# Performance work log

Measured on AMD Instinct MI355X. Metric: run time of the kernel, lower is better.

The kernel has to match this reference:

```python
import jax, jax.numpy as jnp
import numpy as np

BETA = 0.95
NUM_STEPS = 32


def setup_inputs() -> dict:
    key = jax.random.key(0)
    ks = jax.random.split(key, 6)
    B, IN, D, P = 1024, 512, 256, 8
    total = D * P
    x = jax.random.normal(ks[0], (B, IN), jnp.float32)
    W_proj = jax.random.normal(ks[1], (IN, total), jnp.float32) / np.sqrt(IN)
    b_proj = jnp.zeros((total,), jnp.float32)
    # uniform threshold distribution, sorted: linspace(0.5, 2.0, P)
    thresholds = jnp.linspace(0.5, 2.0, P, dtype=jnp.float32)
    rate_W = jax.random.normal(ks[2], (P, 1), jnp.float32) / np.sqrt(P)
    rate_b = jnp.zeros((1,), jnp.float32)
    conv1_w = jax.random.normal(ks[3], (P // 2, P, 3), jnp.float32) / np.sqrt(P * 3)
    conv1_b = jnp.zeros((P // 2,), jnp.float32)
    conv2_w = jax.random.normal(ks[4], (1, P // 2, 1), jnp.float32) / np.sqrt(P // 2)
    conv2_b = jnp.zeros((1,), jnp.float32)
    fusion = jnp.array([0.6, 0.4], jnp.float32)
    return dict(x=x, W_proj=W_proj, b_proj=b_proj, thresholds=thresholds,
                rate_W=rate_W, rate_b=rate_b, conv1_w=conv1_w, conv1_b=conv1_b,
                conv2_w=conv2_w, conv2_b=conv2_b, fusion=fusion)


def _conv1d(x, w, b):
    # x: [N, C_in, T], w: [C_out, C_in, K] -> [N, C_out, T] (SAME padding)
    y = jax.lax.conv_general_dilated(x, w, window_strides=(1,), padding='SAME',
                                     dimension_numbers=('NCH', 'OIH', 'NCH'))
    return y + b[None, :, None]


def reference(x, W_proj, b_proj, thresholds, rate_W, rate_b,
              conv1_w, conv1_b, conv2_w, conv2_b, fusion):
    B = x.shape[0]
    P = thresholds.shape[0]
    D = W_proj.shape[1] // P
    # constant input current per neuron: [B, D, P]
    I = (x @ W_proj + b_proj).reshape(B, D, P)

    # LIF recurrence (snntorch Leaky, reset_mechanism='subtract'):
    #   reset = H(mem_prev - thr); mem = beta*mem_prev + I - reset*thr; spk = H(mem - thr)
    def step(mem, _):
        reset = (mem > thresholds).astype(mem.dtype)
        mem = BETA * mem + I - reset * thresholds
        spk = (mem > thresholds).astype(mem.dtype)
        return mem, spk

    mem0 = jnp.zeros((B, D, P), x.dtype)
    _, spikes = jax.lax.scan(step, mem0, None, length=NUM_STEPS)  # [T, B, D, P]

    # rate branch
    rates = spikes.mean(axis=0)                        # [B, D, P]
    rate_dec = (rates @ rate_W)[..., 0] + rate_b[0]    # [B, D]

    # temporal branch: [B*D, P, T]
    s = jnp.transpose(spikes, (1, 2, 3, 0)).reshape(B * D, P, NUM_STEPS)
    h = jax.nn.relu(_conv1d(s, conv1_w, conv1_b))
    h = _conv1d(h, conv2_w, conv2_b)                   # [B*D, 1, T]
    temp_dec = h.mean(axis=-1).reshape(B, D)

    fw = jax.nn.softmax(fusion)
    return fw[0] * rate_dec + fw[1] * temp_dec
```

## Files before the change

kernel.cpp:

```cpp
#include <hip/hip_runtime.h>
#include <type_traits>


constexpr int IN_DIM  = 512;
constexpr int D_DIM   = 256;
constexpr int NTOT    = 2048;
constexpr int T_STEPS = 32;

constexpr int TM = 64;
constexpr int TN = 64;
constexpr int TK = 32;
constexpr int NSPLIT = 4;
constexpr int KSPLIT = IN_DIM / NSPLIT;

__global__ __launch_bounds__(128, 2)
void popcode_gemm(const float* __restrict__ x,
                  const float* __restrict__ Wp,
                  float* __restrict__ ws)
{
    __shared__ float As[TK][TM + 4];
    __shared__ float Bs[TK][TN];

    const int tid = threadIdx.x;
    const int b0  = blockIdx.x * TM;
    const int c0  = blockIdx.y * TN;
    const int k0  = blockIdx.z * KSPLIT;
    const int rg  = tid >> 3;
    const int dl  = tid & 7;
    const int r4  = rg * 4;

    float acc[4][8];
#pragma unroll
    for (int i = 0; i < 4; ++i)
#pragma unroll
        for (int j = 0; j < 8; ++j) acc[i][j] = 0.f;

    for (int kc = k0; kc < k0 + KSPLIT; kc += TK) {
#pragma unroll
        for (int i = 0; i < 4; ++i) {
            const int f   = tid + 128 * i;
            const int row = f >> 3;
            const int c4  = (f & 7) * 4;
            const float4 v =
                *reinterpret_cast<const float4*>(x + (b0 + row) * IN_DIM + kc + c4);
            As[c4 + 0][row] = v.x;
            As[c4 + 1][row] = v.y;
            As[c4 + 2][row] = v.z;
            As[c4 + 3][row] = v.w;
        }
#pragma unroll
        for (int i = 0; i < 4; ++i) {
            const int f  = tid + 128 * i;
            const int r  = f >> 4;
            const int c4 = (f & 15) * 4;
            *reinterpret_cast<float4*>(&Bs[r][c4]) =
                *reinterpret_cast<const float4*>(Wp + (kc + r) * NTOT + c0 + c4);
        }
        __syncthreads();

#pragma unroll 16
        for (int k = 0; k < TK; ++k) {
            const float4 a = *reinterpret_cast<const float4*>(&As[k][r4]);
            const float4 u = *reinterpret_cast<const float4*>(&Bs[k][dl * 8]);
            const float4 v = *reinterpret_cast<const float4*>(&Bs[k][dl * 8 + 4]);
            const float ar[4] = {a.x, a.y, a.z, a.w};
#pragma unroll
            for (int r = 0; r < 4; ++r) {
                acc[r][0] += ar[r] * u.x;  acc[r][1] += ar[r] * u.y;
                acc[r][2] += ar[r] * u.z;  acc[r][3] += ar[r] * u.w;
                acc[r][4] += ar[r] * v.x;  acc[r][5] += ar[r] * v.y;
                acc[r][6] += ar[r] * v.z;  acc[r][7] += ar[r] * v.w;
            }
        }
        __syncthreads();
    }

    float* dst = ws + (size_t)blockIdx.z * 1024 * NTOT;
#pragma unroll
    for (int bi = 0; bi < 4; ++bi) {
        float* p = dst + (size_t)(b0 + r4 + bi) * NTOT + c0 + dl * 8;
        *reinterpret_cast<float4*>(p)     = {acc[bi][0], acc[bi][1], acc[bi][2], acc[bi][3]};
        *reinterpret_cast<float4*>(p + 4) = {acc[bi][4], acc[bi][5], acc[bi][6], acc[bi][7]};
    }
}

__global__ __launch_bounds__(256)
void popcode_epi(const float* __restrict__ ws,
                 const float* __restrict__ bp,
                 const float* __restrict__ thrs,
                 const float* __restrict__ rateW,
                 const float* __restrict__ rateB,
                 const float* __restrict__ c1w,
                 const float* __restrict__ c1b,
                 const float* __restrict__ c2w,
                 const float* __restrict__ c2b,
                 const float* __restrict__ fus,
                 float* __restrict__ out)
{
    __shared__ float lut[3][256][4];
    __shared__ float rlut[256];
    __shared__ float wlds[96];
    __shared__ uint4 exch[256];

    const int tid = threadIdx.x;
    const int wv  = tid >> 6;
    const int h   = wv & 1;
    const int nl  = ((wv >> 1) << 6) | (tid & 63);
    const int n   = blockIdx.x * 128 + nl;
    const int b   = n >> 8;
    const int d   = n & 255;

    if (tid < 96) wlds[tid] = c1w[tid];
    {
        float rv = 0.f;
#pragma unroll
        for (int p = 0; p < 8; ++p)
            rv += (float)((tid >> p) & 1) * rateW[p];
        rlut[tid] = rv;
    }
    __syncthreads();
#pragma unroll
    for (int i = 0; i < 12; ++i) {
        const int e    = 256 * i + tid;
        const int k    = e >> 10;
        const int byte = (e >> 2) & 255;
        const int c    = e & 3;
        float v = (k == 1) ? c1b[c] : 0.f;
#pragma unroll
        for (int p = 0; p < 8; ++p)
            v = fmaf((float)((byte >> p) & 1), wlds[(c * 8 + p) * 3 + k], v);
        (&lut[0][0][0])[e] = v;
    }

    float w2c[4];
#pragma unroll
    for (int c = 0; c < 4; ++c) w2c[c] = c2w[c];
    const float rb_ = rateB[0];
    const float bb2 = c2b[0];
    const float f0 = fus[0], f1 = fus[1];
    const float fm = fmaxf(f0, f1);
    const float e0 = __expf(f0 - fm), e1 = __expf(f1 - fm);
    const float inv = 1.f / (e0 + e1);
    const float fw0 = e0 * inv, fw1 = e1 * inv;

    const size_t base  = (size_t)b * NTOT + d * 8 + h * 4;
    const size_t slice = (size_t)1024 * NTOT;
    float4 iv = *reinterpret_cast<const float4*>(ws + base);
#pragma unroll
    for (int s = 1; s < NSPLIT; ++s) {
        const float4 q = *reinterpret_cast<const float4*>(ws + s * slice + base);
        iv.x += q.x; iv.y += q.y; iv.z += q.z; iv.w += q.w;
    }
    const float4 bpv = *reinterpret_cast<const float4*>(bp + d * 8 + h * 4);
    const float4 tv  = *reinterpret_cast<const float4*>(thrs + h * 4);
    float Iv[4]  = {iv.x + bpv.x, iv.y + bpv.y, iv.z + bpv.z, iv.w + bpv.w};
    float thr[4] = {tv.x, tv.y, tv.z, tv.w};
    float Imt[4], mem[4];
    bool  spk[4];
#pragma unroll
    for (int p = 0; p < 4; ++p) {
        Imt[p] = Iv[p] - thr[p];
        mem[p] = 0.f;
        spk[p] = false;
    }

    unsigned nib[4] = {0u, 0u, 0u, 0u};
#pragma unroll
    for (int t = 0; t < T_STEPS; ++t) {
        unsigned nb = 0u;
#pragma unroll
        for (int p = 0; p < 4; ++p) {
            mem[p] = 0.95f * mem[p] + (spk[p] ? Imt[p] : Iv[p]);
            spk[p] = mem[p] > thr[p];
            nb |= spk[p] ? (1u << p) : 0u;
        }
        nib[t >> 3] |= nb << (4 * (t & 7));
    }

    __syncthreads();
    exch[tid] = uint4{nib[0], nib[1], nib[2], nib[3]};
    __syncthreads();
    const uint4 pr = exch[tid ^ 64];
    const unsigned prn[4] = {pr.x, pr.y, pr.z, pr.w};
    unsigned lo[4], hi[4];
#pragma unroll
    for (int w = 0; w < 4; ++w) {
        lo[w] = h ? prn[w] : nib[w];
        hi[w] = h ? nib[w] : prn[w];
    }

    auto getbyte = [&](int t) -> unsigned {
        const int w = t >> 3, s = 4 * (t & 7);
        return ((lo[w] >> s) & 15u) | (((hi[w] >> s) & 15u) << 4);
    };
    const float* lutf = &lut[0][0][0];
    float tacc = 0.f, rsum = 0.f;

    auto conv_half = [&](auto T0C) {
        constexpr int T0 = T0C.value;
        unsigned bprev = (T0 == 0) ? 0u : getbyte(T0 - 1);
        unsigned bcur  = getbyte(T0);
#pragma unroll
        for (int i = 0; i < 16; ++i) {
            const int t = T0 + i;
            const unsigned bnext = (t < 31) ? getbyte(t + 1) : 0u;
            const float4 fa = *reinterpret_cast<const float4*>(lutf + bprev * 4);
            const float4 fb = *reinterpret_cast<const float4*>(lutf + 1024 + bcur * 4);
            const float4 fc = *reinterpret_cast<const float4*>(lutf + 2048 + bnext * 4);
            rsum += rlut[bcur];
            const float h0_ = (fa.x + fb.x) + fc.x;
            const float h1_ = (fa.y + fb.y) + fc.y;
            const float h2_ = (fa.z + fb.z) + fc.z;
            const float h3_ = (fa.w + fb.w) + fc.w;
            tacc = fmaf(fmaxf(h0_, 0.f), w2c[0], tacc);
            tacc = fmaf(fmaxf(h1_, 0.f), w2c[1], tacc);
            tacc = fmaf(fmaxf(h2_, 0.f), w2c[2], tacc);
            tacc = fmaf(fmaxf(h3_, 0.f), w2c[3], tacc);
            bprev = bcur;
            bcur  = bnext;
        }
    };
    if (h == 0) conv_half(std::integral_constant<int, 0>{});
    else        conv_half(std::integral_constant<int, 16>{});

    __syncthreads();
    float2* e2 = reinterpret_cast<float2*>(exch);
    e2[tid] = float2{rsum, tacc};
    __syncthreads();
    const float2 q = e2[tid ^ 64];
    rsum += q.x;
    tacc += q.y;

    if (h == 0) {
        const float rdec = rsum * (1.f / 32.f) + rb_;
        const float temp = tacc * (1.f / 32.f) + bb2;
        out[b * D_DIM + d] = fw0 * rdec + fw1 * temp;
    }
}

extern "C" void kernel_launch(void* const* d_in, const int* in_sizes, int n_in,
                              void* d_out, int out_size, void* d_ws, size_t ws_size,
                              hipStream_t stream) {
    const float* x     = (const float*)d_in[0];
    const float* Wp    = (const float*)d_in[1];
    const float* bp    = (const float*)d_in[2];
    const float* thrs  = (const float*)d_in[3];
    const float* rateW = (const float*)d_in[4];
    const float* rateB = (const float*)d_in[5];
    const float* c1w   = (const float*)d_in[6];
    const float* c1b   = (const float*)d_in[7];
    const float* c2w   = (const float*)d_in[8];
    const float* c2b   = (const float*)d_in[9];
    const float* fus   = (const float*)d_in[10];
    float* out = (float*)d_out;
    float* ws  = (float*)d_ws;

    dim3 g1(1024 / TM, NTOT / TN, NSPLIT);
    popcode_gemm<<<g1, dim3(128), 0, stream>>>(x, Wp, ws);

    popcode_epi<<<dim3(2048), dim3(256), 0, stream>>>(
        ws, bp, thrs, rateW, rateB, c1w, c1b, c2w, c2b, fus, out);
}
```

Measured before the change: 123.3 us.

## Replace FP32 SIMT GEMM with split-FP16 MFMA GEMM using async LDS loads

Replaces the split-K FP32 FMA GEMM with a new prep kernel and an MFMA GEMM. The prep kernel splits x and W_proj into high and low FP16 halves, with the low half scaled by 2048, and transposes W. The MFMA kernel runs three f16 MFMAs per tile (hi*hi, lo*hi, hi*lo) to emulate FP32 accuracy, double-buffering tiles via global_load_lds. This removes split-K partial sums and their reduction in the epilogue, but adds an extra prep launch and its memory traffic, and the precision now only approximates FP32.

```diff
diff --git a/kernel.cpp b/kernel.cpp
--- a/kernel.cpp
+++ b/kernel.cpp
@@ -7,85 +7,149 @@
 constexpr int NTOT    = 2048;
 constexpr int T_STEPS = 32;
 
-constexpr int TM = 64;
-constexpr int TN = 64;
-constexpr int TK = 32;
-constexpr int NSPLIT = 4;
-constexpr int KSPLIT = IN_DIM / NSPLIT;
-
-__global__ __launch_bounds__(128, 2)
-void popcode_gemm(const float* __restrict__ x,
-                  const float* __restrict__ Wp,
-                  float* __restrict__ ws)
+typedef _Float16 f16x8 __attribute__((ext_vector_type(8)));
+typedef float    f32x4 __attribute__((ext_vector_type(4)));
+typedef ushort   ushort8 __attribute__((ext_vector_type(8)));
+
+#define GLOBAL_AS __attribute__((address_space(1)))
+#define LDS_AS    __attribute__((address_space(3)))
+
+__device__ __forceinline__ void split_f16(float v, ushort& h, ushort& l) {
+    const _Float16 hf = (_Float16)v;
+    const _Float16 lf = (_Float16)((v - (float)hf) * 2048.0f);
+    h = __builtin_bit_cast(ushort, hf);
+    l = __builtin_bit_cast(ushort, lf);
+}
+
+__global__ __launch_bounds__(256)
+void popcode_prep(const float* __restrict__ x, const float* __restrict__ Wp,
+                  ushort* __restrict__ Ah, ushort* __restrict__ Al,
+                  ushort* __restrict__ Bh, ushort* __restrict__ Bl)
 {
-    __shared__ float As[TK][TM + 4];
-    __shared__ float Bs[TK][TN];
-
-    const int tid = threadIdx.x;
-    const int b0  = blockIdx.x * TM;
-    const int c0  = blockIdx.y * TN;
-    const int k0  = blockIdx.z * KSPLIT;
-    const int rg  = tid >> 3;
-    const int dl  = tid & 7;
-    const int r4  = rg * 4;
-
-    float acc[4][8];
-#pragma unroll
-    for (int i = 0; i < 4; ++i)
-#pragma unroll
-        for (int j = 0; j < 8; ++j) acc[i][j] = 0.f;
-
-    for (int kc = k0; kc < k0 + KSPLIT; kc += TK) {
+    __shared__ float tile[64][68];
+    const int t = threadIdx.x;
+    if (blockIdx.x < 256) {
+        const int idx = (blockIdx.x * 256 + t) * 8;
+        float v[8];
+        *reinterpret_cast<float4*>(v)     = *reinterpret_cast<const float4*>(x + idx);
+        *reinterpret_cast<float4*>(v + 4) = *reinterpret_cast<const float4*>(x + idx + 4);
+        __align__(16) ushort h[8], l[8];
+#pragma unroll
+        for (int j = 0; j < 8; ++j) split_f16(v[j], h[j], l[j]);
+        *reinterpret_cast<ushort8*>(Ah + idx) = *reinterpret_cast<const ushort8*>(h);
+        *reinterpret_cast<ushort8*>(Al + idx) = *reinterpret_cast<const ushort8*>(l);
+    } else {
+        const int ib = blockIdx.x - 256;
+        const int k0 = (ib >> 5) * 64;
+        const int c0 = (ib & 31) * 64;
+        {
+            const int r = t >> 2, cq = (t & 3) * 16;
+#pragma unroll
+            for (int j = 0; j < 4; ++j)
+                *reinterpret_cast<float4*>(&tile[r][cq + j * 4]) =
+                    *reinterpret_cast<const float4*>(Wp + (size_t)(k0 + r) * NTOT + c0 + cq + j * 4);
+        }
+        __syncthreads();
+        const int c = t & 63, kq = (t >> 6) * 16;
+        __align__(16) ushort h[16], l[16];
+#pragma unroll
+        for (int j = 0; j < 16; ++j) split_f16(tile[kq + j][c], h[j], l[j]);
+        ushort* dh = Bh + (size_t)(c0 + c) * 512 + k0 + kq;
+        ushort* dl = Bl + (size_t)(c0 + c) * 512 + k0 + kq;
+        *reinterpret_cast<ushort8*>(dh)     = *reinterpret_cast<const ushort8*>(h);
+        *reinterpret_cast<ushort8*>(dh + 8) = *reinterpret_cast<const ushort8*>(h + 8);
+        *reinterpret_cast<ushort8*>(dl)     = *reinterpret_cast<const ushort8*>(l);
+        *reinterpret_cast<ushort8*>(dl + 8) = *reinterpret_cast<const ushort8*>(l + 8);
+    }
+}
+
+__global__ __launch_bounds__(256, 2)
+void popcode_mfma(const ushort* __restrict__ Ah_g, const ushort* __restrict__ Al_g,
+                  const ushort* __restrict__ Bh_g, const ushort* __restrict__ Bl_g,
+                  float* __restrict__ Iout)
+{
+    __shared__ __align__(16) ushort Lds[2][4][64][32];
+
+    const int tid  = threadIdx.x;
+    const int w    = tid >> 6;
+    const int lane = tid & 63;
+    const int b0   = blockIdx.x * 64;
+    const int c0   = blockIdx.y * 64;
+
+    const ushort* gbase = (w == 0) ? Ah_g : (w == 1) ? Al_g : (w == 2) ? Bh_g : Bl_g;
+    const int     t0    = (w < 2) ? b0 : c0;
+    const int     srow  = lane >> 2;
+    const int     schk  = (lane & 3) * 8;
+
+    const int wr = (w >> 1) * 32;
+    const int wc = (w & 1) * 32;
+    const int lr = lane & 15;
+    const int lg = lane >> 4;
+
+    const f32x4 zero = {0.f, 0.f, 0.f, 0.f};
+    f32x4 acch[2][2] = {{zero, zero}, {zero, zero}};
+    f32x4 accl[2][2] = {{zero, zero}, {zero, zero}};
+
+    LDS_AS char* lds0 = (LDS_AS char*)&Lds[0][0][0][0];
+
+    auto stage = [&](int buf, int kt) {
+        const int koff = kt * 32 + schk;
 #pragma unroll
         for (int i = 0; i < 4; ++i) {
-            const int f   = tid + 128 * i;
-            const int row = f >> 3;
-            const int c4  = (f & 7) * 4;
-            const float4 v =
-                *reinterpret_cast<const float4*>(x + (b0 + row) * IN_DIM + kc + c4);
-            As[c4 + 0][row] = v.x;
-            As[c4 + 1][row] = v.y;
-            As[c4 + 2][row] = v.z;
-            As[c4 + 3][row] = v.w;
-        }
-#pragma unroll
-        for (int i = 0; i < 4; ++i) {
-            const int f  = tid + 128 * i;
-            const int r  = f >> 4;
-            const int c4 = (f & 15) * 4;
-            *reinterpret_cast<float4*>(&Bs[r][c4]) =
-                *reinterpret_cast<const float4*>(Wp + (kc + r) * NTOT + c0 + c4);
-        }
+            const ushort* src = gbase + (size_t)(t0 + srow + 16 * i) * 512 + koff;
+            const int loff = __builtin_amdgcn_readfirstlane(buf * 16384 + w * 4096 + i * 1024);
+            __builtin_amdgcn_global_load_lds((const GLOBAL_AS uint*)src,
+                                             (LDS_AS uint*)(lds0 + loff), 16, 0, 0);
+        }
+    };
+
+    auto compute = [&](int buf) {
+        f16x8 ah[2], al[2], bh[2], bl[2];
+#pragma unroll
+        for (int m = 0; m < 2; ++m) {
+            const int row = wr + m * 16 + lr;
+            ah[m] = *(const f16x8*)&Lds[buf][0][row][lg * 8];
+            al[m] = *(const f16x8*)&Lds[buf][1][row][lg * 8];
+        }
+#pragma unroll
+        for (int n = 0; n < 2; ++n) {
+            const int col = wc + n * 16 + lr;
+            bh[n] = *(const f16x8*)&Lds[buf][2][col][lg * 8];
+            bl[n] = *(const f16x8*)&Lds[buf][3][col][lg * 8];
+        }
+#pragma unroll
+        for (int m = 0; m < 2; ++m)
+#pragma unroll
+            for (int n = 0; n < 2; ++n) {
+                acch[m][n] = __builtin_amdgcn_mfma_f32_16x16x32_f16(ah[m], bh[n], acch[m][n], 0, 0, 0);
+                accl[m][n] = __builtin_amdgcn_mfma_f32_16x16x32_f16(al[m], bh[n], accl[m][n], 0, 0, 0);
+                accl[m][n] = __builtin_amdgcn_mfma_f32_16x16x32_f16(ah[m], bl[n], accl[m][n], 0, 0, 0);
+            }
+    };
+
+    stage(0, 0);
+    __syncthreads();
+    for (int kt = 0; kt < 16; ++kt) {
+        if (kt < 15) stage((kt + 1) & 1, kt + 1);
+        compute(kt & 1);
         __syncthreads();
-
-#pragma unroll 16
-        for (int k = 0; k < TK; ++k) {
-            const float4 a = *reinterpret_cast<const float4*>(&As[k][r4]);
-            const float4 u = *reinterpret_cast<const float4*>(&Bs[k][dl * 8]);
-            const float4 v = *reinterpret_cast<const float4*>(&Bs[k][dl * 8 + 4]);
-            const float ar[4] = {a.x, a.y, a.z, a.w};
-#pragma unroll
-            for (int r = 0; r < 4; ++r) {
-                acc[r][0] += ar[r] * u.x;  acc[r][1] += ar[r] * u.y;
-                acc[r][2] += ar[r] * u.z;  acc[r][3] += ar[r] * u.w;
-                acc[r][4] += ar[r] * v.x;  acc[r][5] += ar[r] * v.y;
-                acc[r][6] += ar[r] * v.z;  acc[r][7] += ar[r] * v.w;
-            }
-        }
-        __syncthreads();
-    }
-
-    float* dst = ws + (size_t)blockIdx.z * 1024 * NTOT;
-#pragma unroll
-    for (int bi = 0; bi < 4; ++bi) {
-        float* p = dst + (size_t)(b0 + r4 + bi) * NTOT + c0 + dl * 8;
-        *reinterpret_cast<float4*>(p)     = {acc[bi][0], acc[bi][1], acc[bi][2], acc[bi][3]};
-        *reinterpret_cast<float4*>(p + 4) = {acc[bi][4], acc[bi][5], acc[bi][6], acc[bi][7]};
-    }
+    }
+
+    const float s = 1.0f / 2048.0f;
+#pragma unroll
+    for (int m = 0; m < 2; ++m)
+#pragma unroll
+        for (int n = 0; n < 2; ++n) {
+            float* dst = Iout + (size_t)(b0 + wr + m * 16 + lg * 4) * NTOT
+                              + c0 + wc + n * 16 + lr;
+#pragma unroll
+            for (int v = 0; v < 4; ++v)
+                dst[(size_t)v * NTOT] = acch[m][n][v] + accl[m][n][v] * s;
+        }
 }
 
 __global__ __launch_bounds__(256)
-void popcode_epi(const float* __restrict__ ws,
+void popcode_epi(const float* __restrict__ Iin,
                  const float* __restrict__ bp,
                  const float* __restrict__ thrs,
                  const float* __restrict__ rateW,
@@ -143,16 +207,10 @@
     const float inv = 1.f / (e0 + e1);
     const float fw0 = e0 * inv, fw1 = e1 * inv;
 
-    const size_t base  = (size_t)b * NTOT + d * 8 + h * 4;
-    const size_t slice = (size_t)1024 * NTOT;
-    float4 iv = *reinterpret_cast<const float4*>(ws + base);
-#pragma unroll
-    for (int s = 1; s < NSPLIT; ++s) {
-        const float4 q = *reinterpret_cast<const float4*>(ws + s * slice + base);
-        iv.x += q.x; iv.y += q.y; iv.z += q.z; iv.w += q.w;
-    }
-    const float4 bpv = *reinterpret_cast<const float4*>(bp + d * 8 + h * 4);
-    const float4 tv  = *reinterpret_cast<const float4*>(thrs + h * 4);
+    const size_t base = (size_t)b * NTOT + d * 8 + h * 4;
+    const float4 iv   = *reinterpret_cast<const float4*>(Iin + base);
+    const float4 bpv  = *reinterpret_cast<const float4*>(bp + d * 8 + h * 4);
+    const float4 tv   = *reinterpret_cast<const float4*>(thrs + h * 4);
     float Iv[4]  = {iv.x + bpv.x, iv.y + bpv.y, iv.z + bpv.z, iv.w + bpv.w};
     float thr[4] = {tv.x, tv.y, tv.z, tv.w};
     float Imt[4], mem[4];
@@ -255,9 +313,14 @@
     float* out = (float*)d_out;
     float* ws  = (float*)d_ws;
 
-    dim3 g1(1024 / TM, NTOT / TN, NSPLIT);
-    popcode_gemm<<<g1, dim3(128), 0, stream>>>(x, Wp, ws);
-
+    ushort* Ah = reinterpret_cast<ushort*>(ws);
+    ushort* Al = Ah + 1024 * 512;
+    ushort* Bh = Al + 1024 * 512;
+    ushort* Bl = Bh + 2048 * 512;
+    float*  I  = ws + 1536 * 1024;
+
+    popcode_prep<<<dim3(512), dim3(256), 0, stream>>>(x, Wp, Ah, Al, Bh, Bl);
+    popcode_mfma<<<dim3(16, 32), dim3(256), 0, stream>>>(Ah, Al, Bh, Bl, I);
     popcode_epi<<<dim3(2048), dim3(256), 0, stream>>>(
-        ws, bp, thrs, rateW, rateB, c1w, c1b, c2w, c2b, fus, out);
-}
+        I, bp, thrs, rateW, rateB, c1w, c1b, c2w, c2b, fus, out);
+}
```

Result: faster. 109.0 us (-11.6%).
